# Performance work log

Measured on AMD Instinct MI355X. Metric: run time of the kernel, lower is better.

The kernel has to match this reference:

```python
import jax, jax.numpy as jnp
import numpy as np

N, IN_C, OUT_C, H, CF = 4096, 256, 256, 8, 6
D = OUT_C // H

def setup_inputs() -> dict:
    key = jax.random.key(0)
    ks = jax.random.split(key, 8)
    x = jax.random.normal(ks[0], (N, IN_C), dtype=jnp.float32)
    positions = jax.random.normal(ks[1], (N, 3), dtype=jnp.float32)
    curv_feats = jax.random.normal(ks[2], (N, CF), dtype=jnp.float32)
    adj = jax.random.randint(ks[3], (N, N), 0, 2, dtype=jnp.int32)
    W = jax.random.normal(ks[4], (OUT_C, IN_C), dtype=jnp.float32) * 0.05
    a_l = jax.random.normal(ks[5], (H, D), dtype=jnp.float32) * 0.1
    a_r = jax.random.normal(ks[6], (H, D), dtype=jnp.float32) * 0.1
    Wc = jax.random.normal(ks[7], (H, CF), dtype=jnp.float32) * 0.1
    gate = jnp.asarray(0.1, dtype=jnp.float32)
    return {"x": x, "positions": positions, "curv_feats": curv_feats,
            "adj": adj, "W": W, "a_l": a_l, "a_r": a_r, "Wc": Wc, "gate": gate}

def reference(x, positions, curv_feats, adj, W, a_l, a_r, Wc, gate):
    n = x.shape[0]
    h = (x @ W.T).reshape(n, H, D)                       # (N,H,D)
    e_l = jnp.einsum('nhd,hd->nh', h, a_l)               # (N,H)
    e_r = jnp.einsum('nhd,hd->nh', h, a_r)               # (N,H)
    logits = jax.nn.leaky_relu(e_l[:, None, :] + e_r[None, :, :], negative_slope=0.2)  # (N,N,H)
    curv_pair = jnp.abs(curv_feats[:, None, :] - curv_feats[None, :, :])  # (N,N,CF)
    curv_bias = jnp.einsum('ijf,hf->ijh', curv_pair, Wc)                  # (N,N,H)
    logits = logits + gate * curv_bias
    mask = (adj > 0)[:, :, None]                          # (N,N,1)
    logits = jnp.where(mask, logits, jnp.float32(-1e9))
    attn = jax.nn.softmax(logits, axis=1)                 # softmax over j (dim=1)
    out = jnp.einsum('ijh,jhd->ihd', attn, h)             # (N,H,D)
    return out.reshape(n, H * D)
```

## Files before the change

kernel.cpp:

```cpp
#include <hip/hip_runtime.h>

#define NN 4096
#define HC 8
#define DC 32
#define OC 256
#define KC 256
#define CF 6

typedef __bf16 bf16_t;
typedef bf16_t bf16x8 __attribute__((ext_vector_type(8)));
typedef float f32x4 __attribute__((ext_vector_type(4)));
typedef float f32x2 __attribute__((ext_vector_type(2)));
typedef unsigned u32x4 __attribute__((ext_vector_type(4)));

#if defined(__has_builtin)
#if __has_builtin(__builtin_amdgcn_exp2f)
#define EXP2F(x) __builtin_amdgcn_exp2f(x)
#else
#define EXP2F(x) exp2f(x)
#endif
#else
#define EXP2F(x) exp2f(x)
#endif

static __device__ __forceinline__ f32x2 unpk(unsigned dw) {
  union { unsigned u; float f; } lo, hi;
  lo.u = dw << 16;
  hi.u = dw & 0xffff0000u;
  return (f32x2){lo.f, hi.f};
}

__global__ __launch_bounds__(256) void prep_all(const float* __restrict__ x,
                                                const float* __restrict__ W,
                                                const float* __restrict__ a_l,
                                                const float* __restrict__ a_r,
                                                const int* __restrict__ adj,
                                                const float* __restrict__ cfeat,
                                                const float* __restrict__ Wc,
                                                const float* __restrict__ gate,
                                                float* __restrict__ e_l2,
                                                bf16_t* __restrict__ erP,
                                                bf16_t* __restrict__ hT2,
                                                unsigned* __restrict__ adjb,
                                                float* __restrict__ cfT,
                                                bf16_t* __restrict__ cfP,
                                                float* __restrict__ Wc2) {
  __shared__ float As[16][68];
  __shared__ float Bs[16][36];
  __shared__ float Ct[DC][65];
  const float LOG2E = 1.44269504088896340736f;
  const int t = threadIdx.x;
  const int bid = blockIdx.x;

  if (bid >= 512) {
    const int pb = bid - 512;
    const int ptid = pb * 256 + t;
    const int lane = t & 63;
    const int wv = pb * 4 + (t >> 6);
    for (int it = 0; it < 32; ++it) {
      int g = wv * 32 + it;
      int i = g >> 6;
      int s = g & 63;
      int v = adj[(size_t)i * NN + s * 64 + lane];
      unsigned long long m = __ballot(v > 0);
      if (lane == 0) *(unsigned long long*)(adjb + i * 128 + s * 2) = m;
    }
    if (ptid < NN * CF) {
      int j = ptid / CF, f = ptid - j * CF;
      float v = cfeat[ptid];
      cfT[f * NN + j] = v;
      int cc = j >> 5, qq = (j >> 3) & 3, tt = j & 7;
      cfP[((cc * 4 + qq) * CF + f) * 8 + tt] = (bf16_t)v;
    }
    if (ptid < HC * CF) Wc2[ptid] = Wc[ptid] * gate[0] * LOG2E;
    return;
  }

  const int i0 = (bid & 63) * 64;
  const int head = bid >> 6;
  const int c0 = head * DC;
  const int tx = t & 7;
  const int ty = t >> 3;
  const int lr = t >> 2;
  const int lk = (t & 3) * 4;

  float acc[2][4] = {};
  for (int kk = 0; kk < KC; kk += 16) {
    f32x4 av = *(const f32x4*)&x[(size_t)(i0 + lr) * KC + kk + lk];
    f32x4 wv;
    if (t < 128) wv = *(const f32x4*)&W[(size_t)(c0 + (t >> 2)) * KC + kk + lk];
    __syncthreads();
    As[lk + 0][lr] = av[0]; As[lk + 1][lr] = av[1];
    As[lk + 2][lr] = av[2]; As[lk + 3][lr] = av[3];
    if (t < 128) {
      int br = t >> 2;
      Bs[lk + 0][br] = wv[0]; Bs[lk + 1][br] = wv[1];
      Bs[lk + 2][br] = wv[2]; Bs[lk + 3][br] = wv[3];
    }
    __syncthreads();
#pragma unroll
    for (int k = 0; k < 16; ++k) {
      f32x2 a = *(const f32x2*)&As[k][ty * 2];
      f32x4 b = *(const f32x4*)&Bs[k][tx * 4];
#pragma unroll
      for (int r = 0; r < 2; ++r)
#pragma unroll
        for (int u = 0; u < 4; ++u)
          acc[r][u] += a[r] * b[u];
    }
  }

  f32x4 al4 = *(const f32x4*)&a_l[c0 + tx * 4];
  f32x4 ar4 = *(const f32x4*)&a_r[c0 + tx * 4];
#pragma unroll
  for (int r = 0; r < 2; ++r) {
    float el = acc[r][0] * al4[0] + acc[r][1] * al4[1] +
               acc[r][2] * al4[2] + acc[r][3] * al4[3];
    float er = acc[r][0] * ar4[0] + acc[r][1] * ar4[1] +
               acc[r][2] * ar4[2] + acc[r][3] * ar4[3];
    el += __shfl_xor(el, 1, 64); el += __shfl_xor(el, 2, 64); el += __shfl_xor(el, 4, 64);
    er += __shfl_xor(er, 1, 64); er += __shfl_xor(er, 2, 64); er += __shfl_xor(er, 4, 64);
    if (tx == 0) {
      int j = i0 + ty * 2 + r;
      e_l2[j * HC + head] = el * LOG2E;
      int cc = j >> 5, qq = (j >> 3) & 3, tt = j & 7;
      erP[((cc * 4 + qq) * HC + head) * 8 + tt] = (bf16_t)(er * LOG2E);
    }
  }

#pragma unroll
  for (int r = 0; r < 2; ++r)
#pragma unroll
    for (int u = 0; u < 4; ++u)
      Ct[tx * 4 + u][ty * 2 + r] = acc[r][u];
  __syncthreads();
  const size_t base = (size_t)head * (NN / 32) * 1024 + (size_t)(bid & 63) * 2048;
#pragma unroll
  for (int rep = 0; rep < 8; ++rep) {
    int idx = rep * 256 + t;
    int dd = (idx >> 3) & 31;
    int jl = (idx >> 10) * 32 + ((idx >> 8) & 3) * 8 + (idx & 7);
    hT2[base + idx] = (bf16_t)Ct[dd][jl];
  }
}

__global__ __launch_bounds__(256, 4) void attn(const unsigned* __restrict__ adjb,
                                               const float* __restrict__ e_l2,
                                               const float* __restrict__ cfT,
                                               const float* __restrict__ Wc2,
                                               const u32x4* __restrict__ cfP4,
                                               const u32x4* __restrict__ erP4,
                                               const bf16_t* __restrict__ hT2,
                                               float* __restrict__ out) {
  __shared__ float Obuf[16][64];
  __shared__ float Sbuf[16][2];
  const int tid = threadIdx.x;
  const int w = tid >> 6;
  const int lane = tid & 63;
  const int il = lane & 15;
  const int quad = lane >> 4;
  const int ibase = blockIdx.x * 16;
  const int hg = blockIdx.y;
  const int i = ibase + il;

  for (int idx = tid; idx < 16 * 64; idx += 256) (&Obuf[0][0])[idx] = 0.f;
  if (tid < 32) (&Sbuf[0][0])[tid] = 0.f;
  __syncthreads();

  f32x2 cfi2[CF];
#pragma unroll
  for (int f = 0; f < CF; ++f) { float v = cfT[f * NN + i]; cfi2[f] = (f32x2){v, v}; }
  f32x2 el2[2];
  {
    f32x2 e0 = *(const f32x2*)&e_l2[i * HC + hg * 2];
#pragma unroll
    for (int u = 0; u < 2; ++u) el2[u] = (f32x2){e0[u], e0[u]};
  }
  float wc[2][CF];
#pragma unroll
  for (int h = 0; h < 2; ++h)
#pragma unroll
    for (int f = 0; f < CF; ++f) wc[h][f] = Wc2[(hg * 2 + h) * CF + f];

  f32x4 acc[2][2];
#pragma unroll
  for (int h = 0; h < 2; ++h)
#pragma unroll
    for (int d = 0; d < 2; ++d) acc[h][d] = (f32x4){0.f, 0.f, 0.f, 0.f};
  f32x2 S2[2];
#pragma unroll
  for (int h = 0; h < 2; ++h) S2[h] = (f32x2){0.f, 0.f};

  const bf16_t* hTbase = hT2 + (size_t)hg * 2 * ((NN / 32) * 1024) + quad * 256 + il * 8;
  const u32x4* cfb = cfP4 + quad * CF;
  const u32x4* erb = erP4 + quad * HC + hg * 2;
  const unsigned* adjrow = adjb + i * 128;

  u32x4 cfc[CF];
#pragma unroll
  for (int f = 0; f < CF; ++f) cfc[f] = cfb[w * (4 * CF) + f];
  u32x4 erc[2];
#pragma unroll
  for (int h = 0; h < 2; ++h) erc[h] = erb[w * (4 * HC) + h];
  unsigned mc = adjrow[w];

  for (int c = w; c < NN / 32; c += 4) {
    const bf16_t* bp0 = hTbase + c * 1024;
    const bf16_t* bp1 = bp0 + (NN / 32) * 1024;
    bf16x8 b00 = *(const bf16x8*)bp0;
    bf16x8 b01 = *(const bf16x8*)(bp0 + 128);
    bf16x8 b10 = *(const bf16x8*)bp1;
    bf16x8 b11 = *(const bf16x8*)(bp1 + 128);

    f32x2 arg[2][4];
#pragma unroll
    for (int h = 0; h < 2; ++h)
#pragma unroll
      for (int p = 0; p < 4; ++p) {
        f32x2 s = el2[h] + unpk(erc[h][p]);
        arg[h][p] = __builtin_elementwise_max(s, 0.2f * s);
      }
#pragma unroll
    for (int f = 0; f < CF; ++f) {
#pragma unroll
      for (int p = 0; p < 4; ++p) {
        f32x2 d2 = cfi2[f] - unpk(cfc[f][p]);
        f32x2 ab = __builtin_elementwise_max(d2, -d2);
#pragma unroll
        for (int h = 0; h < 2; ++h) {
          f32x2 wsp = (f32x2){wc[h][f], wc[h][f]};
          arg[h][p] = __builtin_elementwise_fma(ab, wsp, arg[h][p]);
        }
      }
    }

    const int cn = (c + 4) & (NN / 32 - 1);
    const unsigned m8 = (mc >> (quad * 8)) & 0xffu;
#pragma unroll
    for (int f = 0; f < CF; ++f) cfc[f] = cfb[cn * (4 * CF) + f];
#pragma unroll
    for (int h = 0; h < 2; ++h) erc[h] = erb[cn * (4 * HC) + h];
    mc = adjrow[cn];

    f32x2 mf2[4];
#pragma unroll
    for (int p = 0; p < 4; ++p)
      mf2[p] = (f32x2){(float)((m8 >> (2 * p)) & 1u), (float)((m8 >> (2 * p + 1)) & 1u)};

#pragma unroll
    for (int h = 0; h < 2; ++h) {
      bf16x8 af;
#pragma unroll
      for (int p = 0; p < 4; ++p) {
        f32x2 pv = (f32x2){EXP2F(arg[h][p][0]), EXP2F(arg[h][p][1])};
        pv = pv * mf2[p];
        S2[h] += pv;
        af[2 * p] = (bf16_t)pv[0];
        af[2 * p + 1] = (bf16_t)pv[1];
      }
      acc[h][0] = __builtin_amdgcn_mfma_f32_16x16x32_bf16(af, h ? b10 : b00, acc[h][0], 0, 0, 0);
      acc[h][1] = __builtin_amdgcn_mfma_f32_16x16x32_bf16(af, h ? b11 : b01, acc[h][1], 0, 0, 0);
    }
  }

#pragma unroll
  for (int h = 0; h < 2; ++h) {
    float v = S2[h][0] + S2[h][1];
    v += __shfl_xor(v, 16, 64);
    v += __shfl_xor(v, 32, 64);
    if (quad == 0) atomicAdd(&Sbuf[il][h], v);
  }
#pragma unroll
  for (int h = 0; h < 2; ++h)
#pragma unroll
    for (int dh = 0; dh < 2; ++dh)
#pragma unroll
      for (int r = 0; r < 4; ++r)
        atomicAdd(&Obuf[quad * 4 + r][h * DC + dh * 16 + il], acc[h][dh][r]);
  __syncthreads();

  for (int idx = tid; idx < 16 * 64; idx += 256) {
    int row = idx >> 6;
    int colg = idx & 63;
    out[(size_t)(ibase + row) * OC + hg * 64 + colg] =
        Obuf[row][colg] / Sbuf[row][colg >> 5];
  }
}

extern "C" void kernel_launch(void* const* d_in, const int* in_sizes, int n_in,
                              void* d_out, int out_size, void* d_ws, size_t ws_size,
                              hipStream_t stream) {
  const float* x    = (const float*)d_in[0];
  const float* cfeat= (const float*)d_in[2];
  const int*   adj  = (const int*)d_in[3];
  const float* W    = (const float*)d_in[4];
  const float* a_l  = (const float*)d_in[5];
  const float* a_r  = (const float*)d_in[6];
  const float* Wc   = (const float*)d_in[7];
  const float* gate = (const float*)d_in[8];
  float* out = (float*)d_out;

  char* ws = (char*)d_ws;
  bf16_t*   hT2  = (bf16_t*)ws;
  unsigned* adjb = (unsigned*)(ws + (2u << 20));
  float*    e_l2 = (float*)(ws + (4u << 20));
  float*    cfT  = (float*)(ws + (4u << 20) + (128u << 10));
  float*    Wc2  = (float*)(ws + (4u << 20) + (256u << 10));
  bf16_t*   cfP  = (bf16_t*)(ws + (4u << 20) + (320u << 10));
  bf16_t*   erP  = (bf16_t*)(ws + (4u << 20) + (384u << 10));

  prep_all<<<2560, 256, 0, stream>>>(x, W, a_l, a_r, adj, cfeat, Wc, gate,
                                     e_l2, erP, hT2, adjb, cfT, cfP, Wc2);
  attn<<<dim3(NN / 16, 4), 256, 0, stream>>>(adjb, e_l2, cfT, Wc2,
                                             (const u32x4*)cfP, (const u32x4*)erP,
                                             hT2, out);
}
```

Measured before the change: 228.3 us.

## Double-buffer V operand in LDS via async global_load_lds prefetch

The attention kernel no longer loads the bf16 hT tiles for the MFMA B operand straight into registers each iteration. Each wave now prefetches the next chunk into a per-wave double-buffered LDS region using global_load_lds DMA and reads the current chunk from LDS. The aim is to hide global load latency behind the logit and exp computation. In exchange it adds 32KB of LDS per block, which may limit occupancy, plus extra LDS read traffic, and it relies on the compiler placing the right wait counts for the DMA writes.

```diff
diff --git a/kernel.cpp b/kernel.cpp
--- a/kernel.cpp
+++ b/kernel.cpp
@@ -12,6 +12,9 @@
 typedef float f32x4 __attribute__((ext_vector_type(4)));
 typedef float f32x2 __attribute__((ext_vector_type(2)));
 typedef unsigned u32x4 __attribute__((ext_vector_type(4)));
+
+#define AS1 __attribute__((address_space(1)))
+#define AS3 __attribute__((address_space(3)))
 
 #if defined(__has_builtin)
 #if __has_builtin(__builtin_amdgcn_exp2f)
@@ -154,6 +157,7 @@
                                                float* __restrict__ out) {
   __shared__ float Obuf[16][64];
   __shared__ float Sbuf[16][2];
+  __shared__ __align__(16) char vbuf[4][2][4096];
   const int tid = threadIdx.x;
   const int w = tid >> 6;
   const int lane = tid & 63;
@@ -196,6 +200,15 @@
   const u32x4* erb = erP4 + quad * HC + hg * 2;
   const unsigned* adjrow = adjb + i * 128;
 
+  {
+    const bf16_t* p0 = hTbase + w * 1024;
+    const bf16_t* p1 = p0 + (NN / 32) * 1024;
+    char* lb = &vbuf[w][0][0];
+    __builtin_amdgcn_global_load_lds((const AS1 void*)p0,         (AS3 void*)(lb),        16, 0, 0);
+    __builtin_amdgcn_global_load_lds((const AS1 void*)(p0 + 128), (AS3 void*)(lb + 1024), 16, 0, 0);
+    __builtin_amdgcn_global_load_lds((const AS1 void*)p1,         (AS3 void*)(lb + 2048), 16, 0, 0);
+    __builtin_amdgcn_global_load_lds((const AS1 void*)(p1 + 128), (AS3 void*)(lb + 3072), 16, 0, 0);
+  }
   u32x4 cfc[CF];
 #pragma unroll
   for (int f = 0; f < CF; ++f) cfc[f] = cfb[w * (4 * CF) + f];
@@ -204,13 +217,13 @@
   for (int h = 0; h < 2; ++h) erc[h] = erb[w * (4 * HC) + h];
   unsigned mc = adjrow[w];
 
+  int par = 0;
   for (int c = w; c < NN / 32; c += 4) {
-    const bf16_t* bp0 = hTbase + c * 1024;
-    const bf16_t* bp1 = bp0 + (NN / 32) * 1024;
-    bf16x8 b00 = *(const bf16x8*)bp0;
-    bf16x8 b01 = *(const bf16x8*)(bp0 + 128);
-    bf16x8 b10 = *(const bf16x8*)bp1;
-    bf16x8 b11 = *(const bf16x8*)(bp1 + 128);
+    const char* lbr = &vbuf[w][par][0];
+    bf16x8 b00 = *(const bf16x8*)(lbr + lane * 16);
+    bf16x8 b01 = *(const bf16x8*)(lbr + 1024 + lane * 16);
+    bf16x8 b10 = *(const bf16x8*)(lbr + 2048 + lane * 16);
+    bf16x8 b11 = *(const bf16x8*)(lbr + 3072 + lane * 16);
 
     f32x2 arg[2][4];
 #pragma unroll
@@ -236,6 +249,15 @@
 
     const int cn = (c + 4) & (NN / 32 - 1);
     const unsigned m8 = (mc >> (quad * 8)) & 0xffu;
+    {
+      const bf16_t* p0 = hTbase + cn * 1024;
+      const bf16_t* p1 = p0 + (NN / 32) * 1024;
+      char* lb = &vbuf[w][par ^ 1][0];
+      __builtin_amdgcn_global_load_lds((const AS1 void*)p0,         (AS3 void*)(lb),        16, 0, 0);
+      __builtin_amdgcn_global_load_lds((const AS1 void*)(p0 + 128), (AS3 void*)(lb + 1024), 16, 0, 0);
+      __builtin_amdgcn_global_load_lds((const AS1 void*)p1,         (AS3 void*)(lb + 2048), 16, 0, 0);
+      __builtin_amdgcn_global_load_lds((const AS1 void*)(p1 + 128), (AS3 void*)(lb + 3072), 16, 0, 0);
+    }
 #pragma unroll
     for (int f = 0; f < CF; ++f) cfc[f] = cfb[cn * (4 * CF) + f];
 #pragma unroll
@@ -261,6 +283,7 @@
       acc[h][0] = __builtin_amdgcn_mfma_f32_16x16x32_bf16(af, h ? b10 : b00, acc[h][0], 0, 0, 0);
       acc[h][1] = __builtin_amdgcn_mfma_f32_16x16x32_bf16(af, h ? b11 : b01, acc[h][1], 0, 0, 0);
     }
+    par ^= 1;
   }
 
 #pragma unroll
```

After: 228.0 us. About the same (-0.1%).
